# Performance work log

Measured on AMD Instinct MI355X. Metric: run time of the kernel, lower is better.

The kernel has to match this reference:

```python
import jax, jax.numpy as jnp
import numpy as np

N_HEAD = 16
SCALE = True
NEG = 10000.0


def setup_inputs() -> dict:
    key = jax.random.key(0)
    ks = jax.random.split(key, 5)
    B, S, D = 4, 1024, 1024
    x = jax.random.normal(ks[0], (B, S, D), dtype=jnp.float32)
    # GPT-2 Conv1D weights: W has shape [in, out], init ~N(0, 0.02)
    w_attn = jax.random.normal(ks[1], (D, 3 * D), dtype=jnp.float32) * 0.02
    b_attn = jnp.zeros((3 * D,), dtype=jnp.float32)
    w_proj = jax.random.normal(ks[2], (D, D), dtype=jnp.float32) * 0.02
    b_proj = jnp.zeros((D,), dtype=jnp.float32)
    return {"x": x, "w_attn": w_attn, "b_attn": b_attn,
            "w_proj": w_proj, "b_proj": b_proj}


def reference(x, w_attn, b_attn, w_proj, b_proj):
    B, S, D = x.shape
    H = N_HEAD
    hd = D // H
    # c_attn: Conv1D == x @ W + b
    qkv = jnp.einsum('bsd,de->bse', x, w_attn) + b_attn
    q, k, v = jnp.split(qkv, 3, axis=-1)
    # split heads -> [B, H, S, hd]
    q = q.reshape(B, S, H, hd).transpose(0, 2, 1, 3)
    k = k.reshape(B, S, H, hd).transpose(0, 2, 1, 3)
    v = v.reshape(B, S, H, hd).transpose(0, 2, 1, 3)
    # scores [B, H, S, S]
    w = jnp.einsum('bhqd,bhkd->bhqk', q, k)
    if SCALE:
        w = w / jnp.sqrt(jnp.float32(hd))
    # multiplicative causal mask: w*b - 10000*(1-b)
    bmask = jnp.tril(jnp.ones((S, S), dtype=w.dtype))[None, None]
    w = w * bmask - NEG * (1.0 - bmask)
    w = jax.nn.softmax(w, axis=-1)
    # attn_pdrop = 0 -> dropout is identity
    a = jnp.einsum('bhqk,bhkd->bhqd', w, v)
    # merge heads
    a = a.transpose(0, 2, 1, 3).reshape(B, S, D)
    # c_proj; resid_pdrop = 0
    out = jnp.einsum('bsd,de->bse', a, w_proj) + b_proj
    return out
```

## Files before the change

### kernel.cpp

```cpp
#include <hip/hip_runtime.h>
#include <hip/hip_bf16.h>


typedef __bf16 bf16x8 __attribute__((ext_vector_type(8)));
typedef __bf16 bf16x4 __attribute__((ext_vector_type(4)));
typedef float f32x4 __attribute__((ext_vector_type(4)));

__device__ __forceinline__ void load_lds16(const void* g, void* l) {
  __builtin_amdgcn_global_load_lds(
      (const __attribute__((address_space(1))) void*)g,
      (__attribute__((address_space(3))) void*)l, 16, 0, 0);
}

#define BAR8 asm volatile("s_barrier" ::: "memory")
#define LGKM0 asm volatile("s_waitcnt lgkmcnt(0)" ::: "memory")

__global__ __launch_bounds__(256) void prep(
    const float* __restrict__ x, const float* __restrict__ w_attn,
    const float* __restrict__ w_proj, __bf16* __restrict__ Xb,
    __bf16* __restrict__ WT_attn, __bf16* __restrict__ WT_proj) {
  __shared__ __bf16 tile[32][33];
  const int blk = blockIdx.x;
  const int tid = threadIdx.x;
  if (blk < 4096) {
    const float* W;
    __bf16* WT;
    int n0, k0, N;
    if (blk < 3072) {
      W = w_attn; WT = WT_attn; N = 3072;
      n0 = (blk % 96) * 32; k0 = (blk / 96) * 32;
    } else {
      W = w_proj; WT = WT_proj; N = 1024;
      const int t = blk - 3072;
      n0 = (t & 31) * 32; k0 = (t >> 5) * 32;
    }
    const int tx = tid & 31, ty = tid >> 5;
#pragma unroll
    for (int j = 0; j < 32; j += 8)
      tile[ty + j][tx] = (__bf16)W[(size_t)(k0 + ty + j) * N + n0 + tx];
    __syncthreads();
#pragma unroll
    for (int j = 0; j < 32; j += 8)
      WT[(size_t)(n0 + ty + j) * 1024 + k0 + tx] = tile[tx][ty + j];
  } else {
    const size_t i = (size_t)(blk - 4096) * 4096 + tid * 16;
    const float4* xp = (const float4*)(x + i);
    float4 a = xp[0], b = xp[1], c = xp[2], d = xp[3];
    bf16x8 o0, o1;
    o0[0] = (__bf16)a.x; o0[1] = (__bf16)a.y; o0[2] = (__bf16)a.z; o0[3] = (__bf16)a.w;
    o0[4] = (__bf16)b.x; o0[5] = (__bf16)b.y; o0[6] = (__bf16)b.z; o0[7] = (__bf16)b.w;
    o1[0] = (__bf16)c.x; o1[1] = (__bf16)c.y; o1[2] = (__bf16)c.z; o1[3] = (__bf16)c.w;
    o1[4] = (__bf16)d.x; o1[5] = (__bf16)d.y; o1[6] = (__bf16)d.z; o1[7] = (__bf16)d.w;
    *(bf16x8*)(Xb + i) = o0;
    *(bf16x8*)(Xb + i + 8) = o1;
  }
}


#define STG(GMAT, GROW0, K0, LOFF)                                             \
  _Pragma("unroll") for (int i_ = 0; i_ < 2; ++i_)                             \
    load_lds16((GMAT) + (size_t)((GROW0) + i_ * 64 + wave * 8 + srow) * 1024 + \
                   (K0) + schunk * 8,                                          \
               smem8 + (LOFF) + (i_ * 64 + wave * 8) * 64);

#define LDA8(BASE, MH)                                                         \
  _Pragma("unroll") for (int m_ = 0; m_ < 4; ++m_)                             \
  _Pragma("unroll") for (int kk_ = 0; kk_ < 2; ++kk_)                          \
    af[m_][kk_] = *(const bf16x8*)((BASE) + ((MH)*64 + m_ * 16 + l16) * 64 +   \
                                   (((kk_ * 4 + quad) ^ rsw) * 8));

#define LDB8(BASE, NLO)                                                        \
  _Pragma("unroll") for (int n_ = 0; n_ < 2; ++n_)                             \
  _Pragma("unroll") for (int kk_ = 0; kk_ < 2; ++kk_)                          \
    bf[(NLO) + n_][kk_] =                                                      \
        *(const bf16x8*)((BASE) + ((waveN & 1) * 64 + ((NLO) + n_) * 16 +      \
                                   l16) * 64 +                                 \
                         (((kk_ * 4 + quad) ^ rsw) * 8));

#define MFMA_HALF(MH, NLO)                                                     \
  __builtin_amdgcn_s_setprio(1);                                               \
  _Pragma("unroll") for (int m_ = 0; m_ < 4; ++m_)                             \
  _Pragma("unroll") for (int n_ = 0; n_ < 2; ++n_) {                           \
    acc[(MH)*4 + m_][(NLO) + n_] = __builtin_amdgcn_mfma_f32_16x16x32_bf16(    \
        af[m_][0], bf[(NLO) + n_][0], acc[(MH)*4 + m_][(NLO) + n_], 0, 0, 0);  \
    acc[(MH)*4 + m_][(NLO) + n_] = __builtin_amdgcn_mfma_f32_16x16x32_bf16(    \
        af[m_][1], bf[(NLO) + n_][1], acc[(MH)*4 + m_][(NLO) + n_], 0, 0, 0);  \
  }                                                                            \
  __builtin_amdgcn_s_setprio(0);

__global__ __launch_bounds__(512, 2) void gemm_qkv8(
    const __bf16* __restrict__ A, const __bf16* __restrict__ BT,
    const float* __restrict__ bias, __bf16* __restrict__ Qp,
    __bf16* __restrict__ Kp, __bf16* __restrict__ Vt) {
  __shared__ __bf16 smem8[65536];
  const int tid = threadIdx.x;
  const int lane = tid & 63;
  const int wave = tid >> 6;
  const int waveM = wave >> 2;
  const int waveN = wave & 3;
  const int l16 = lane & 15;
  const int quad = lane >> 4;
  const int rsw = l16 & 7;
  const int srow = lane >> 3;
  const int schunk = (lane & 7) ^ srow;

  const int bid = blockIdx.x;
  const int c = bid & 7, l = bid >> 3;
  const int tm = (c >> 1) * 4 + l / 6;
  const int tn = (c & 1) * 6 + l % 6;
  const int rowBase = tm * 256;
  const int colBase = tn * 256;

  const __bf16* aRd = smem8 + waveM * 8192;
  const __bf16* bRd = smem8 + 16384 + (waveN >> 1) * 8192;

  f32x4 acc[8][4] = {};
  bf16x8 af[4][2], bf[4][2];

  STG(A, rowBase, 0, 0);
  STG(A, rowBase + 128, 0, 8192);
  STG(BT, colBase, 0, 16384);
  STG(BT, colBase + 128, 0, 24576);
  STG(BT, colBase, 64, 32768 + 16384);
  STG(BT, colBase + 128, 64, 32768 + 24576);
  STG(A, rowBase, 64, 32768);
  asm volatile("s_waitcnt vmcnt(6)" ::: "memory");
  BAR8;

  for (int t = 0; t < 8; ++t) {
    const int kO = t * 128 + 64;
    const int kS2 = t * 128 + 128;
    const int kS3 = t * 128 + 192;
    const bool s2 = kS2 < 1024;
    const bool s3 = kS3 < 1024;

    LDA8(aRd, 0);
    LDB8(bRd, 0);
    STG(A, rowBase + 128, kO, 32768 + 8192);
    BAR8; LGKM0;
    MFMA_HALF(0, 0);
    BAR8;

    LDB8(bRd, 2);
    BAR8; LGKM0;
    MFMA_HALF(0, 2);
    BAR8;

    LDA8(aRd, 1);
    if (s2) { STG(BT, colBase, kS2, 16384); }
    BAR8; LGKM0;
    MFMA_HALF(1, 2);
    BAR8;

    if (s2) {
      STG(BT, colBase + 128, kS2, 24576);
      STG(A, rowBase, kS2, 0);
      asm volatile("s_waitcnt vmcnt(6)" ::: "memory");
    } else {
      asm volatile("s_waitcnt vmcnt(0)" ::: "memory");
    }
    BAR8;
    MFMA_HALF(1, 0);
    BAR8;

    LDA8(aRd + 32768, 0);
    LDB8(bRd + 32768, 0);
    if (s2) { STG(A, rowBase + 128, kS2, 8192); }
    BAR8; LGKM0;
    MFMA_HALF(0, 0);
    BAR8;

    LDB8(bRd + 32768, 2);
    BAR8; LGKM0;
    MFMA_HALF(0, 2);
    BAR8;

    LDA8(aRd + 32768, 1);
    if (s3) { STG(BT, colBase, kS3, 32768 + 16384); }
    BAR8; LGKM0;
    MFMA_HALF(1, 2);
    BAR8;

    if (s3) {
      STG(BT, colBase + 128, kS3, 32768 + 24576);
      STG(A, rowBase, kS3, 32768);
    }
    asm volatile("s_waitcnt vmcnt(6)" ::: "memory");
    BAR8;
    MFMA_HALF(1, 0);
    BAR8;
  }

  const int seg = colBase >> 10;
  if (seg == 2) {
#pragma unroll
    for (int mm = 0; mm < 8; ++mm) {
      const int r0 = waveM * 128 + mm * 16 + quad * 4;
#pragma unroll
      for (int n = 0; n < 4; ++n) {
        const int cR = waveN * 64 + n * 16 + l16;
        const float bv = bias[colBase + cR];
        bf16x4 pk;
#pragma unroll
        for (int r = 0; r < 4; ++r) pk[r] = (__bf16)(acc[mm][n][r] + bv);
        *(bf16x4*)(&smem8[cR * 256 + (r0 ^ (l16 << 4))]) = pk;
      }
    }
    __syncthreads();
    const int b_ = rowBase >> 10;
    const int s0 = rowBase & 1023;
    const int hBase = (colBase & 1023) >> 6;
    const int ch = lane & 31;
#pragma unroll
    for (int p = 0; p < 16; ++p) {
      const int c2 = p * 16 + wave * 2 + (lane >> 5);
      bf16x8 v =
          *(const bf16x8*)(&smem8[c2 * 256 + ((ch * 8) ^ ((c2 & 15) << 4))]);
      const int bhd = (b_ * 16 + hBase + (c2 >> 6)) * 64 + (c2 & 63);
      *(bf16x8*)(&Vt[(size_t)bhd * 1024 + s0 + ch * 8]) = v;
    }
  } else {
#pragma unroll
    for (int mm = 0; mm < 8; ++mm) {
      const int row0 = rowBase + waveM * 128 + mm * 16 + quad * 4;
#pragma unroll
      for (int n = 0; n < 4; ++n) {
        const int col = colBase + waveN * 64 + n * 16 + l16;
        const float bv = bias[col];
        const int cc = col & 1023;
        __bf16* dst = (seg == 0) ? Qp : Kp;
#pragma unroll
        for (int r = 0; r < 4; ++r) {
          const int row = row0 + r;
          const float v = acc[mm][n][r] + bv;
          const int bh = ((row >> 10) << 4) + (cc >> 6);
          dst[((size_t)bh << 16) + (size_t)(row & 1023) * 64 + (cc & 63)] =
              (__bf16)v;
        }
      }
    }
  }
}

__global__ __launch_bounds__(256) void gemm_out(
    const __bf16* __restrict__ A, const __bf16* __restrict__ BT,
    const float* __restrict__ bias, float* __restrict__ C) {
  __shared__ __bf16 sA[3][128 * 32];
  __shared__ __bf16 sB[3][128 * 32];
  const int tid = threadIdx.x;
  const int lane = tid & 63;
  const int wave = tid >> 6;
  const int waveM = wave >> 1, waveN = wave & 1;
  const int quad = lane >> 4;
  const int l16 = lane & 15;
  const int rowBase = blockIdx.x * 128;
  const int colBase = blockIdx.y * 128;
  const int rIn = lane >> 2;
  const int sIn = lane & 3;
  const int gc = sIn ^ (rIn & 3) ^ ((rIn >> 2) & 3);
  const int readSlot = quad ^ (l16 & 3) ^ ((l16 >> 2) & 3);
  f32x4 acc[4][4] = {};

#define GO_STAGE(bi, k0_)                                                      \
  _Pragma("unroll") for (int j_ = 0; j_ < 2; ++j_) {                           \
    const int rb = wave * 32 + j_ * 16;                                        \
    load_lds16(&A[(size_t)(rowBase + rb + rIn) * 1024 + (k0_) + gc * 8],       \
               &sA[bi][rb * 32]);                                              \
    load_lds16(&BT[(size_t)(colBase + rb + rIn) * 1024 + (k0_) + gc * 8],      \
               &sB[bi][rb * 32]);                                              \
  }

  GO_STAGE(0, 0);
  GO_STAGE(1, 32);
  asm volatile("s_waitcnt vmcnt(4)" ::: "memory");
  BAR8;

#pragma unroll
  for (int i = 0; i < 32; ++i) {
    if (i + 2 < 32) { GO_STAGE((i + 2) % 3, (i + 2) * 32); }
    const __bf16* sAc = sA[i % 3];
    const __bf16* sBc = sB[i % 3];
    bf16x8 af[4], bfr[4];
#pragma unroll
    for (int mt = 0; mt < 4; ++mt)
      af[mt] = *(const bf16x8*)(&sAc[(waveM * 64 + mt * 16 + l16) * 32 +
                                     readSlot * 8]);
#pragma unroll
    for (int nt = 0; nt < 4; ++nt)
      bfr[nt] = *(const bf16x8*)(&sBc[(waveN * 64 + nt * 16 + l16) * 32 +
                                      readSlot * 8]);
    __builtin_amdgcn_s_setprio(1);
#pragma unroll
    for (int mt = 0; mt < 4; ++mt)
#pragma unroll
      for (int nt = 0; nt < 4; ++nt)
        acc[mt][nt] = __builtin_amdgcn_mfma_f32_16x16x32_bf16(
            af[mt], bfr[nt], acc[mt][nt], 0, 0, 0);
    __builtin_amdgcn_s_setprio(0);
    if (i + 1 < 32) {
      if (i + 2 < 32) {
        asm volatile("s_waitcnt vmcnt(4)" ::: "memory");
      } else {
        asm volatile("s_waitcnt vmcnt(0)" ::: "memory");
      }
      BAR8;
    }
  }

#pragma unroll
  for (int mt = 0; mt < 4; ++mt) {
    const int row = rowBase + waveM * 64 + mt * 16 + quad * 4;
#pragma unroll
    for (int nt = 0; nt < 4; ++nt) {
      const int col = colBase + waveN * 64 + nt * 16 + l16;
      const float bv = bias[col];
#pragma unroll
      for (int r = 0; r < 4; ++r)
        C[(size_t)(row + r) * 1024 + col] = acc[mt][nt][r] + bv;
    }
  }
}

__global__ __launch_bounds__(512, 4) void attn_mfma(
    const __bf16* __restrict__ Qp, const __bf16* __restrict__ Kp,
    const __bf16* __restrict__ VT, __bf16* __restrict__ Aout) {
  __shared__ __bf16 sK[2][128 * 64];
  __shared__ __bf16 sV[2][64 * 128];
  __shared__ __bf16 sP[8 * 16 * 64];

  const int tid = threadIdx.x;
  const int lane = tid & 63;
  const int wave = tid >> 6;
  const int wq = wave & 3;
  const int tileSel = wave >> 2;
  const int quad = lane >> 4;
  const int l16 = lane & 15;
  const int swq = l16 & 7;

  const int bh = blockIdx.x & 63;
  const int pr = blockIdx.x >> 6;
  const int b = bh >> 4, h = bh & 15;
  const int qbB = (15 - pr) * 64, qbA = pr * 64;
  const int ktB_max = (15 - pr) >> 1, ktA_max = pr >> 1;
  const int myQb = tileSel ? qbA : qbB;
  const int myKt = tileSel ? ktA_max : ktB_max;

  const __bf16* Qb = Qp + ((size_t)bh << 16);
  const __bf16* Kb = Kp + ((size_t)bh << 16);
  const __bf16* VTb = VT + (size_t)bh * 64 * 1024;

  bf16x8 qA0, qA1;
  {
    const __bf16* qr = Qb + (size_t)(myQb + wq * 16 + l16) * 64 + quad * 8;
    qA0 = *(const bf16x8*)qr;
    qA1 = *(const bf16x8*)(qr + 32);
  }

  f32x4 O[4] = {};
  float ps[4] = {0.f, 0.f, 0.f, 0.f};
  __bf16* pw = sP + wave * 1024;

#define ATTN_STAGE(bi, kbase)                                                  \
  _Pragma("unroll") for (int i_ = 0; i_ < 2; ++i_) {                           \
    const int rb = wave * 16 + i_ * 8;                                         \
    load_lds16(Kb + (size_t)((kbase) + rb + (lane >> 3)) * 64 +                \
                   (((lane & 7) ^ ((lane >> 3) & 7)) << 3),                    \
               &sK[bi][rb * 64]);                                              \
  }                                                                            \
  _Pragma("unroll") for (int i_ = 0; i_ < 2; ++i_) {                           \
    const int db = wave * 8 + i_ * 4;                                          \
    const int d = db + (lane >> 4);                                            \
    load_lds16(VTb + (size_t)d * 1024 + (kbase) +                              \
                   (((lane & 15) ^ (d & 7)) << 3),                             \
               &sV[bi][db * 128]);                                             \
  }

  ATTN_STAGE(0, 0);
  asm volatile("s_waitcnt vmcnt(0)" ::: "memory");
  BAR8;

  for (int kt = 0; kt <= ktB_max; ++kt) {
    const int kb = kt * 128;
    const int cur = kt & 1;
    if (kt < ktB_max) { ATTN_STAGE(cur ^ 1, kb + 128); }

    if (kt <= myKt) {
      const __bf16* skc = sK[cur];
      const __bf16* svc = sV[cur];

      float sc[8][4];
      __builtin_amdgcn_s_setprio(1);
#pragma unroll
      for (int n = 0; n < 8; ++n) {
        const int key = n * 16 + l16;
        bf16x8 kB0 = *(const bf16x8*)(&skc[key * 64 + ((quad ^ swq) << 3)]);
        bf16x8 kB1 = *(const bf16x8*)(&skc[key * 64 + (((quad + 4) ^ swq) << 3)]);
        f32x4 cacc = {};
        cacc = __builtin_amdgcn_mfma_f32_16x16x32_bf16(qA0, kB0, cacc, 0, 0, 0);
        cacc = __builtin_amdgcn_mfma_f32_16x16x32_bf16(qA1, kB1, cacc, 0, 0, 0);
#pragma unroll
        for (int r = 0; r < 4; ++r) sc[n][r] = cacc[r] * 0.125f;
      }
      __builtin_amdgcn_s_setprio(0);

      if (kt == myKt) {
#pragma unroll
        for (int n = 0; n < 8; ++n) {
          const int kg = kb + n * 16 + l16;
#pragma unroll
          for (int r = 0; r < 4; ++r)
            if (kg > myQb + wq * 16 + quad * 4 + r) sc[n][r] = -1.0e30f;
        }
      }

#pragma unroll
      for (int n = 0; n < 8; ++n)
#pragma unroll
        for (int r = 0; r < 4; ++r) {
          float p = __expf(fminf(sc[n][r], 60.0f));
          sc[n][r] = p;
          ps[r] += p;
        }

      const int kb8 = l16 >> 3, lo = l16 & 7;
#pragma unroll
      for (int hf = 0; hf < 2; ++hf) {
#pragma unroll
        for (int n = 4 * hf; n < 4 * hf + 4; ++n) {
          const int crel = (n - 4 * hf) * 2 + kb8;
#pragma unroll
          for (int r = 0; r < 4; ++r) {
            const int q = quad * 4 + r;
            pw[q * 64 + ((crel ^ (q & 7)) << 3) + lo] = (__bf16)sc[n][r];
          }
        }
        __builtin_amdgcn_s_setprio(1);
#pragma unroll
        for (int cc = 2 * hf; cc < 2 * hf + 2; ++cc) {
          const int crel = (cc - 2 * hf) * 4 + quad;
          bf16x8 pA = *(const bf16x8*)(&pw[l16 * 64 + ((crel ^ swq) << 3)]);
#pragma unroll
          for (int nt = 0; nt < 4; ++nt) {
            bf16x8 vB = *(const bf16x8*)(&svc[(nt * 16 + l16) * 128 +
                                              (((cc * 4 + quad) ^ swq) << 3)]);
            O[nt] = __builtin_amdgcn_mfma_f32_16x16x32_bf16(pA, vB, O[nt], 0, 0, 0);
          }
        }
        __builtin_amdgcn_s_setprio(0);
      }
    }

    if (kt < ktB_max) {
      asm volatile("s_waitcnt vmcnt(0)" ::: "memory");
      BAR8;
    }
  }

  float inv[4];
#pragma unroll
  for (int r = 0; r < 4; ++r) {
    float pa = ps[r];
    pa += __shfl_xor(pa, 1);
    pa += __shfl_xor(pa, 2);
    pa += __shfl_xor(pa, 4);
    pa += __shfl_xor(pa, 8);
    inv[r] = 1.0f / pa;
  }
#pragma unroll
  for (int nt = 0; nt < 4; ++nt) {
#pragma unroll
    for (int r = 0; r < 4; ++r) {
      const int q = myQb + wq * 16 + quad * 4 + r;
      Aout[((size_t)b * 1024 + q) * 1024 + h * 64 + nt * 16 + l16] =
          (__bf16)(O[nt][r] * inv[r]);
    }
  }
}

extern "C" void kernel_launch(void* const* d_in, const int* in_sizes, int n_in,
                              void* d_out, int out_size, void* d_ws,
                              size_t ws_size, hipStream_t stream) {
  const float* x      = (const float*)d_in[0];
  const float* w_attn = (const float*)d_in[1];
  const float* b_attn = (const float*)d_in[2];
  const float* w_proj = (const float*)d_in[3];
  const float* b_proj = (const float*)d_in[4];
  float* out = (float*)d_out;

  char* ws = (char*)d_ws;
  __bf16* WT_attn = (__bf16*)(ws);
  __bf16* WT_proj = (__bf16*)(ws + 6291456);
  __bf16* Xb      = (__bf16*)(ws + 8388608);
  __bf16* Qp      = (__bf16*)(ws + 16777216);
  __bf16* Kp      = (__bf16*)(ws + 25165824);
  __bf16* VT      = (__bf16*)(ws + 33554432);
  __bf16* Aattn   = (__bf16*)(ws + 41943040);

  prep<<<5120, 256, 0, stream>>>(x, w_attn, w_proj, Xb, WT_attn, WT_proj);
  gemm_qkv8<<<192, 512, 0, stream>>>(Xb, WT_attn, b_attn, Qp, Kp, VT);
  attn_mfma<<<512, 512, 0, stream>>>(Qp, Kp, VT, Aattn);
  gemm_out<<<dim3(32, 8), 256, 0, stream>>>(Aattn, WT_proj, b_proj, out);
}
```

Before: 163.5 us.

## Replace pipelined 256x256 QKV GEMM with simple 128x128 single-buffer kernel

Swaps the eight-wave, double-buffered 256x256-tile QKV GEMM with staged LDS prefetch for a four-wave 128x128-tile kernel. The new kernel loads a 32-wide K slice per iteration with two block barriers. The V-transpose epilogue is redone in two 64-column halves through a smaller LDS buffer. This cuts LDS use and register pressure and gives a larger grid, but it drops load/compute overlap and halves per-block data reuse.

Result: no change. 165.2 us (+1.0%).

```diff
diff --git a/kernel.cpp b/kernel.cpp
--- a/kernel.cpp
+++ b/kernel.cpp
@@ -13,7 +13,6 @@
 }
 
 #define BAR8 asm volatile("s_barrier" ::: "memory")
-#define LGKM0 asm volatile("s_waitcnt lgkmcnt(0)" ::: "memory")
 
 __global__ __launch_bounds__(256) void prep(
     const float* __restrict__ x, const float* __restrict__ w_attn,
@@ -56,183 +55,104 @@
   }
 }
 
-
-#define STG(GMAT, GROW0, K0, LOFF)                                             \
-  _Pragma("unroll") for (int i_ = 0; i_ < 2; ++i_)                             \
-    load_lds16((GMAT) + (size_t)((GROW0) + i_ * 64 + wave * 8 + srow) * 1024 + \
-                   (K0) + schunk * 8,                                          \
-               smem8 + (LOFF) + (i_ * 64 + wave * 8) * 64);
-
-#define LDA8(BASE, MH)                                                         \
-  _Pragma("unroll") for (int m_ = 0; m_ < 4; ++m_)                             \
-  _Pragma("unroll") for (int kk_ = 0; kk_ < 2; ++kk_)                          \
-    af[m_][kk_] = *(const bf16x8*)((BASE) + ((MH)*64 + m_ * 16 + l16) * 64 +   \
-                                   (((kk_ * 4 + quad) ^ rsw) * 8));
-
-#define LDB8(BASE, NLO)                                                        \
-  _Pragma("unroll") for (int n_ = 0; n_ < 2; ++n_)                             \
-  _Pragma("unroll") for (int kk_ = 0; kk_ < 2; ++kk_)                          \
-    bf[(NLO) + n_][kk_] =                                                      \
-        *(const bf16x8*)((BASE) + ((waveN & 1) * 64 + ((NLO) + n_) * 16 +      \
-                                   l16) * 64 +                                 \
-                         (((kk_ * 4 + quad) ^ rsw) * 8));
-
-#define MFMA_HALF(MH, NLO)                                                     \
-  __builtin_amdgcn_s_setprio(1);                                               \
-  _Pragma("unroll") for (int m_ = 0; m_ < 4; ++m_)                             \
-  _Pragma("unroll") for (int n_ = 0; n_ < 2; ++n_) {                           \
-    acc[(MH)*4 + m_][(NLO) + n_] = __builtin_amdgcn_mfma_f32_16x16x32_bf16(    \
-        af[m_][0], bf[(NLO) + n_][0], acc[(MH)*4 + m_][(NLO) + n_], 0, 0, 0);  \
-    acc[(MH)*4 + m_][(NLO) + n_] = __builtin_amdgcn_mfma_f32_16x16x32_bf16(    \
-        af[m_][1], bf[(NLO) + n_][1], acc[(MH)*4 + m_][(NLO) + n_], 0, 0, 0);  \
-  }                                                                            \
-  __builtin_amdgcn_s_setprio(0);
-
-__global__ __launch_bounds__(512, 2) void gemm_qkv8(
+__global__ __launch_bounds__(256) void gemm_qkv(
     const __bf16* __restrict__ A, const __bf16* __restrict__ BT,
     const float* __restrict__ bias, __bf16* __restrict__ Qp,
     __bf16* __restrict__ Kp, __bf16* __restrict__ Vt) {
-  __shared__ __bf16 smem8[65536];
+  __shared__ __bf16 smem[8192];
+  __bf16* sA = smem;
+  __bf16* sB = smem + 4096;
   const int tid = threadIdx.x;
   const int lane = tid & 63;
   const int wave = tid >> 6;
-  const int waveM = wave >> 2;
-  const int waveN = wave & 3;
+  const int waveM = wave >> 1, waveN = wave & 1;
+  const int quad = lane >> 4;
   const int l16 = lane & 15;
-  const int quad = lane >> 4;
-  const int rsw = l16 & 7;
-  const int srow = lane >> 3;
-  const int schunk = (lane & 7) ^ srow;
-
-  const int bid = blockIdx.x;
-  const int c = bid & 7, l = bid >> 3;
-  const int tm = (c >> 1) * 4 + l / 6;
-  const int tn = (c & 1) * 6 + l % 6;
-  const int rowBase = tm * 256;
-  const int colBase = tn * 256;
-
-  const __bf16* aRd = smem8 + waveM * 8192;
-  const __bf16* bRd = smem8 + 16384 + (waveN >> 1) * 8192;
-
-  f32x4 acc[8][4] = {};
-  bf16x8 af[4][2], bf[4][2];
-
-  STG(A, rowBase, 0, 0);
-  STG(A, rowBase + 128, 0, 8192);
-  STG(BT, colBase, 0, 16384);
-  STG(BT, colBase + 128, 0, 24576);
-  STG(BT, colBase, 64, 32768 + 16384);
-  STG(BT, colBase + 128, 64, 32768 + 24576);
-  STG(A, rowBase, 64, 32768);
-  asm volatile("s_waitcnt vmcnt(6)" ::: "memory");
-  BAR8;
-
-  for (int t = 0; t < 8; ++t) {
-    const int kO = t * 128 + 64;
-    const int kS2 = t * 128 + 128;
-    const int kS3 = t * 128 + 192;
-    const bool s2 = kS2 < 1024;
-    const bool s3 = kS3 < 1024;
-
-    LDA8(aRd, 0);
-    LDB8(bRd, 0);
-    STG(A, rowBase + 128, kO, 32768 + 8192);
-    BAR8; LGKM0;
-    MFMA_HALF(0, 0);
-    BAR8;
-
-    LDB8(bRd, 2);
-    BAR8; LGKM0;
-    MFMA_HALF(0, 2);
-    BAR8;
-
-    LDA8(aRd, 1);
-    if (s2) { STG(BT, colBase, kS2, 16384); }
-    BAR8; LGKM0;
-    MFMA_HALF(1, 2);
-    BAR8;
-
-    if (s2) {
-      STG(BT, colBase + 128, kS2, 24576);
-      STG(A, rowBase, kS2, 0);
-      asm volatile("s_waitcnt vmcnt(6)" ::: "memory");
-    } else {
-      asm volatile("s_waitcnt vmcnt(0)" ::: "memory");
-    }
-    BAR8;
-    MFMA_HALF(1, 0);
-    BAR8;
-
-    LDA8(aRd + 32768, 0);
-    LDB8(bRd + 32768, 0);
-    if (s2) { STG(A, rowBase + 128, kS2, 8192); }
-    BAR8; LGKM0;
-    MFMA_HALF(0, 0);
-    BAR8;
-
-    LDB8(bRd + 32768, 2);
-    BAR8; LGKM0;
-    MFMA_HALF(0, 2);
-    BAR8;
-
-    LDA8(aRd + 32768, 1);
-    if (s3) { STG(BT, colBase, kS3, 32768 + 16384); }
-    BAR8; LGKM0;
-    MFMA_HALF(1, 2);
-    BAR8;
-
-    if (s3) {
-      STG(BT, colBase + 128, kS3, 32768 + 24576);
-      STG(A, rowBase, kS3, 32768);
-    }
-    asm volatile("s_waitcnt vmcnt(6)" ::: "memory");
-    BAR8;
-    MFMA_HALF(1, 0);
-    BAR8;
+  const int rowBase = blockIdx.y * 128;
+  const int colBase = blockIdx.x * 128;
+  const int rIn = lane >> 2;
+  const int sIn = lane & 3;
+  const int gc = sIn ^ (rIn & 3) ^ ((rIn >> 2) & 3);
+  const int readSlot = quad ^ (l16 & 3) ^ ((l16 >> 2) & 3);
+  f32x4 acc[4][4] = {};
+
+  for (int k0 = 0; k0 < 1024; k0 += 32) {
+    __syncthreads();
+#pragma unroll
+    for (int j = 0; j < 2; ++j) {
+      const int rb = wave * 32 + j * 16;
+      load_lds16(&A[(size_t)(rowBase + rb + rIn) * 1024 + k0 + gc * 8],
+                 &sA[rb * 32]);
+      load_lds16(&BT[(size_t)(colBase + rb + rIn) * 1024 + k0 + gc * 8],
+                 &sB[rb * 32]);
+    }
+    __syncthreads();
+    bf16x8 af[4], bfr[4];
+#pragma unroll
+    for (int mt = 0; mt < 4; ++mt)
+      af[mt] = *(const bf16x8*)(&sA[(waveM * 64 + mt * 16 + l16) * 32 +
+                                    readSlot * 8]);
+#pragma unroll
+    for (int nt = 0; nt < 4; ++nt)
+      bfr[nt] = *(const bf16x8*)(&sB[(waveN * 64 + nt * 16 + l16) * 32 +
+                                     readSlot * 8]);
+#pragma unroll
+    for (int mt = 0; mt < 4; ++mt)
+#pragma unroll
+      for (int nt = 0; nt < 4; ++nt)
+        acc[mt][nt] = __builtin_amdgcn_mfma_f32_16x16x32_bf16(
+            af[mt], bfr[nt], acc[mt][nt], 0, 0, 0);
   }
 
   const int seg = colBase >> 10;
   if (seg == 2) {
-#pragma unroll
-    for (int mm = 0; mm < 8; ++mm) {
-      const int r0 = waveM * 128 + mm * 16 + quad * 4;
-#pragma unroll
-      for (int n = 0; n < 4; ++n) {
-        const int cR = waveN * 64 + n * 16 + l16;
-        const float bv = bias[colBase + cR];
-        bf16x4 pk;
-#pragma unroll
-        for (int r = 0; r < 4; ++r) pk[r] = (__bf16)(acc[mm][n][r] + bv);
-        *(bf16x4*)(&smem8[cR * 256 + (r0 ^ (l16 << 4))]) = pk;
-      }
-    }
-    __syncthreads();
     const int b_ = rowBase >> 10;
     const int s0 = rowBase & 1023;
-    const int hBase = (colBase & 1023) >> 6;
-    const int ch = lane & 31;
-#pragma unroll
-    for (int p = 0; p < 16; ++p) {
-      const int c2 = p * 16 + wave * 2 + (lane >> 5);
-      bf16x8 v =
-          *(const bf16x8*)(&smem8[c2 * 256 + ((ch * 8) ^ ((c2 & 15) << 4))]);
-      const int bhd = (b_ * 16 + hBase + (c2 >> 6)) * 64 + (c2 & 63);
-      *(bf16x8*)(&Vt[(size_t)bhd * 1024 + s0 + ch * 8]) = v;
+    __syncthreads();
+#pragma unroll
+    for (int h = 0; h < 2; ++h) {
+      if (waveN == h) {
+#pragma unroll
+        for (int nt = 0; nt < 4; ++nt) {
+          const int cRel = nt * 16 + l16;
+          const float bv = bias[colBase + h * 64 + cRel];
+#pragma unroll
+          for (int mt = 0; mt < 4; ++mt) {
+            const int rb4 = waveM * 64 + mt * 16 + quad * 4;
+            bf16x4 pk;
+#pragma unroll
+            for (int r = 0; r < 4; ++r) pk[r] = (__bf16)(acc[mt][nt][r] + bv);
+            *(bf16x4*)(&smem[cRel * 128 + (rb4 ^ (l16 << 3))]) = pk;
+          }
+        }
+      }
+      __syncthreads();
+#pragma unroll
+      for (int p = 0; p < 4; ++p) {
+        const int g = p * 256 + tid;
+        const int cRel = g >> 4, ch = g & 15;
+        bf16x8 v =
+            *(const bf16x8*)(&smem[cRel * 128 + ((ch * 8) ^ ((cRel & 15) << 3))]);
+        const int cc = (colBase + h * 64 + cRel) & 1023;
+        const int bhd = (b_ * 16 + (cc >> 6)) * 64 + (cc & 63);
+        *(bf16x8*)(&Vt[(size_t)bhd * 1024 + s0 + ch * 8]) = v;
+      }
+      __syncthreads();
     }
   } else {
-#pragma unroll
-    for (int mm = 0; mm < 8; ++mm) {
-      const int row0 = rowBase + waveM * 128 + mm * 16 + quad * 4;
-#pragma unroll
-      for (int n = 0; n < 4; ++n) {
-        const int col = colBase + waveN * 64 + n * 16 + l16;
+    __bf16* dst = (seg == 0) ? Qp : Kp;
+#pragma unroll
+    for (int mt = 0; mt < 4; ++mt) {
+      const int row0 = rowBase + waveM * 64 + mt * 16 + quad * 4;
+#pragma unroll
+      for (int nt = 0; nt < 4; ++nt) {
+        const int col = colBase + waveN * 64 + nt * 16 + l16;
         const float bv = bias[col];
         const int cc = col & 1023;
-        __bf16* dst = (seg == 0) ? Qp : Kp;
 #pragma unroll
         for (int r = 0; r < 4; ++r) {
           const int row = row0 + r;
-          const float v = acc[mm][n][r] + bv;
+          const float v = acc[mt][nt][r] + bv;
           const int bh = ((row >> 10) << 4) + (cc >> 6);
           dst[((size_t)bh << 16) + (size_t)(row & 1023) * 64 + (cc & 63)] =
               (__bf16)v;
@@ -497,7 +417,7 @@
   __bf16* Aattn   = (__bf16*)(ws + 41943040);
 
   prep<<<5120, 256, 0, stream>>>(x, w_attn, w_proj, Xb, WT_attn, WT_proj);
-  gemm_qkv8<<<192, 512, 0, stream>>>(Xb, WT_attn, b_attn, Qp, Kp, VT);
+  gemm_qkv<<<dim3(24, 32), 256, 0, stream>>>(Xb, WT_attn, b_attn, Qp, Kp, VT);
   attn_mfma<<<512, 512, 0, stream>>>(Qp, Kp, VT, Aattn);
   gemm_out<<<dim3(32, 8), 256, 0, stream>>>(Aattn, WT_proj, b_proj, out);
 }
```
